# Optimization experiments

Measured on AMD Instinct MI355X. Metric: run time of the kernel, lower is better.

Reference implementation:

```python
import jax, jax.numpy as jnp
import numpy as np


def _decode(fm):
    # fm: [B, A, H, W, 5+C] YOLO head output
    B, A, H, W, D = fm.shape
    box = fm[..., :4].reshape(B, -1, 4)
    conf = jax.nn.sigmoid(fm[..., 4].reshape(B, -1))
    cls = jax.nn.sigmoid(fm[..., 5:].reshape(B, -1, D - 5))
    # Faithful to the torch in-place sequence:
    #   b0 = (b0 - b2/2)*W ; b1 = (b1 - b3/2)*H
    #   b2 = (NEW b0 + OLD b2/2)*W ; b3 = (NEW b1 + OLD b3/2)*H
    w = jnp.asarray(W, fm.dtype)
    h = jnp.asarray(H, fm.dtype)
    x1 = (box[..., 0] - box[..., 2] / 2) * w
    y1 = (box[..., 1] - box[..., 3] / 2) * h
    x2 = (x1 + box[..., 2] / 2) * w
    y2 = (y1 + box[..., 3] / 2) * h
    boxes = jnp.stack([x1, y1, x2, y2], axis=-1)  # [B, A*H*W, 4]
    return boxes, conf, cls


def setup_inputs() -> dict:
    key = jax.random.key(0)
    k0, k1, k2, k3 = jax.random.split(key, 4)
    B, A, C = 16, 3, 80
    fm0 = jax.random.uniform(k0, (B, A, 80, 80, 5 + C), dtype=jnp.float32)
    fm1 = jax.random.uniform(k1, (B, A, 40, 40, 5 + C), dtype=jnp.float32)
    fm2 = jax.random.uniform(k2, (B, A, 20, 20, 5 + C), dtype=jnp.float32)
    detection_targets = jax.random.uniform(k3, (1, 4), dtype=jnp.float32)
    return {"fm0": fm0, "fm1": fm1, "fm2": fm2,
            "detection_targets": detection_targets}


def reference(fm0, fm1, fm2, detection_targets):
    boxes, scores, classes = [], [], []
    for fm in (fm0, fm1, fm2):
        b, s, c = _decode(fm)
        boxes.append(b)
        scores.append(s)
        classes.append(c)
    all_boxes = jnp.concatenate(boxes, axis=1)    # [B, N, 4]
    all_scores = jnp.concatenate(scores, axis=1)  # [B, N]
    all_classes = jnp.concatenate(classes, axis=1)  # [B, N, C]
    # Pack like the torch nms_input: [x1, y1, x2, y2, conf, cls...]
    return jnp.concatenate(
        [all_boxes, all_scores[..., None], all_classes], axis=-1)  # [B, N, 5+C]
```

## Files before the change

### kernel.cpp

```cpp
#include <hip/hip_runtime.h>

#define NROWS_OUT 25200
#define L0_FLOATS 26112000
#define L1_FLOATS 6528000
#define L2_FLOATS 1632000
#define TOTAL_FLOATS (L0_FLOATS + L1_FLOATS + L2_FLOATS)
#define TOTAL4   (TOTAL_FLOATS / 4)
#define HALF4    (TOTAL4 / 2)

typedef float v4f __attribute__((ext_vector_type(4)));

__device__ __forceinline__ float fast_sigmoid(float x) {
    float e = __expf(-x);
    return __builtin_amdgcn_rcpf(1.0f + e);
}

template <int ROWS, int OFF, int SCALE>
__device__ __forceinline__ void process4(const float* __restrict__ in,
                                         float* __restrict__ out,
                                         int f_local) {
    constexpr int ROWS85 = ROWS * 85;
    const int b   = f_local / ROWS85;
    const int rem = f_local - b * ROWS85;
    const int c0  = rem % 85;

    int g = f_local;
    if (c0 <= 3)  g = f_local - c0;
    if (c0 >= 82) g = f_local + (85 - c0);

    const v4f x = *(const v4f*)(in + f_local);
    const float r0 = in[g + 0];
    const float r1 = in[g + 1];
    const float r2 = in[g + 2];
    const float r3 = in[g + 3];

    const float sc = (float)SCALE;
    const float h2 = 0.5f * r2, h3 = 0.5f * r3;
    const float q0 = (r0 - h2) * sc;
    const float q1 = (r1 - h3) * sc;
    const float q2 = (q0 + h2) * sc;
    const float q3 = (q1 + h3) * sc;

    float xv[4] = {x.x, x.y, x.z, x.w};
    float y[4];
#pragma unroll
    for (int k = 0; k < 4; ++k) {
        int c = c0 + k;
        if (c >= 85) c -= 85;
        const float s = fast_sigmoid(xv[k]);
        const float q = (c == 0) ? q0 : ((c == 1) ? q1 : ((c == 2) ? q2 : q3));
        y[k] = (c < 4) ? q : s;
    }

    const int out_f = (b * NROWS_OUT + OFF) * 85 + rem;
    v4f yo; yo.x = y[0]; yo.y = y[1]; yo.z = y[2]; yo.w = y[3];
    __builtin_nontemporal_store(yo, (v4f*)(out + out_f));
}

__device__ __forceinline__ void dispatch4(const float* __restrict__ fm0,
                                          const float* __restrict__ fm1,
                                          const float* __restrict__ fm2,
                                          float* __restrict__ out, int f) {
    if (f < L0_FLOATS) {
        process4<19200, 0, 80>(fm0, out, f);
    } else if (f < L0_FLOATS + L1_FLOATS) {
        process4<4800, 19200, 40>(fm1, out, f - L0_FLOATS);
    } else {
        process4<1200, 24000, 20>(fm2, out, f - (L0_FLOATS + L1_FLOATS));
    }
}

__global__ __launch_bounds__(256) void yolo_decode_kernel(
    const float* __restrict__ fm0, const float* __restrict__ fm1,
    const float* __restrict__ fm2, float* __restrict__ out) {
    const int v = blockIdx.x * 256 + threadIdx.x;
    if (v >= HALF4) return;
    dispatch4(fm0, fm1, fm2, out, v * 4);
    dispatch4(fm0, fm1, fm2, out, (v + HALF4) * 4);
}

extern "C" void kernel_launch(void* const* d_in, const int* in_sizes, int n_in,
                              void* d_out, int out_size, void* d_ws, size_t ws_size,
                              hipStream_t stream) {
    const float* fm0 = (const float*)d_in[0];
    const float* fm1 = (const float*)d_in[1];
    const float* fm2 = (const float*)d_in[2];
    float* out = (float*)d_out;

    const int blocks = (HALF4 + 255) / 256;
    hipLaunchKernelGGL(yolo_decode_kernel, dim3(blocks), dim3(256), 0, stream,
                       fm0, fm1, fm2, out);
}
```

Measured before the change: 236.3 us.

## Split decode into bulk sigmoid stream kernel and per-row box fixup kernel

```diff
diff --git a/kernel.cpp b/kernel.cpp
--- a/kernel.cpp
+++ b/kernel.cpp
@@ -1,12 +1,17 @@
 #include <hip/hip_runtime.h>
 
 #define NROWS_OUT 25200
+#define ROWS0 19200
+#define ROWS1 4800
+#define ROWS2 1200
+#define NB 16
 #define L0_FLOATS 26112000
 #define L1_FLOATS 6528000
 #define L2_FLOATS 1632000
 #define TOTAL_FLOATS (L0_FLOATS + L1_FLOATS + L2_FLOATS)
 #define TOTAL4   (TOTAL_FLOATS / 4)
 #define HALF4    (TOTAL4 / 2)
+#define NROWS_TOT (NB * NROWS_OUT)
 
 typedef float v4f __attribute__((ext_vector_type(4)));
 
@@ -15,24 +20,53 @@
     return __builtin_amdgcn_rcpf(1.0f + e);
 }
 
+template <int ROWS, int OFF>
+__device__ __forceinline__ void stream4(const float* __restrict__ in,
+                                        float* __restrict__ out,
+                                        int f_local) {
+    constexpr int ROWS85 = ROWS * 85;
+    const int b = f_local / ROWS85;
+    const v4f x = *(const v4f*)(in + f_local);
+    v4f y;
+    y.x = fast_sigmoid(x.x);
+    y.y = fast_sigmoid(x.y);
+    y.z = fast_sigmoid(x.z);
+    y.w = fast_sigmoid(x.w);
+    const int out_f = f_local + (b * (NROWS_OUT - ROWS) + OFF) * 85;
+    __builtin_nontemporal_store(y, (v4f*)(out + out_f));
+}
+
+__device__ __forceinline__ void sdispatch(const float* __restrict__ fm0,
+                                          const float* __restrict__ fm1,
+                                          const float* __restrict__ fm2,
+                                          float* __restrict__ out, int f) {
+    if (f < L0_FLOATS) {
+        stream4<ROWS0, 0>(fm0, out, f);
+    } else if (f < L0_FLOATS + L1_FLOATS) {
+        stream4<ROWS1, ROWS0>(fm1, out, f - L0_FLOATS);
+    } else {
+        stream4<ROWS2, ROWS0 + ROWS1>(fm2, out, f - (L0_FLOATS + L1_FLOATS));
+    }
+}
+
+__global__ __launch_bounds__(256) void yolo_sigmoid_kernel(
+    const float* __restrict__ fm0, const float* __restrict__ fm1,
+    const float* __restrict__ fm2, float* __restrict__ out) {
+    const int v = blockIdx.x * 256 + threadIdx.x;
+    if (v >= HALF4) return;
+    sdispatch(fm0, fm1, fm2, out, v * 4);
+    sdispatch(fm0, fm1, fm2, out, (v + HALF4) * 4);
+}
+
 template <int ROWS, int OFF, int SCALE>
-__device__ __forceinline__ void process4(const float* __restrict__ in,
-                                         float* __restrict__ out,
-                                         int f_local) {
-    constexpr int ROWS85 = ROWS * 85;
-    const int b   = f_local / ROWS85;
-    const int rem = f_local - b * ROWS85;
-    const int c0  = rem % 85;
-
-    int g = f_local;
-    if (c0 <= 3)  g = f_local - c0;
-    if (c0 >= 82) g = f_local + (85 - c0);
-
-    const v4f x = *(const v4f*)(in + f_local);
-    const float r0 = in[g + 0];
-    const float r1 = in[g + 1];
-    const float r2 = in[g + 2];
-    const float r3 = in[g + 3];
+__device__ __forceinline__ void fixrow(const float* __restrict__ in,
+                                       float* __restrict__ out, int tloc) {
+    const int b = tloc / ROWS;
+    const int gin = tloc * 85;
+    const float r0 = in[gin + 0];
+    const float r1 = in[gin + 1];
+    const float r2 = in[gin + 2];
+    const float r3 = in[gin + 3];
 
     const float sc = (float)SCALE;
     const float h2 = 0.5f * r2, h3 = 0.5f * r3;
@@ -41,42 +75,25 @@
     const float q2 = (q0 + h2) * sc;
     const float q3 = (q1 + h3) * sc;
 
-    float xv[4] = {x.x, x.y, x.z, x.w};
-    float y[4];
-#pragma unroll
-    for (int k = 0; k < 4; ++k) {
-        int c = c0 + k;
-        if (c >= 85) c -= 85;
-        const float s = fast_sigmoid(xv[k]);
-        const float q = (c == 0) ? q0 : ((c == 1) ? q1 : ((c == 2) ? q2 : q3));
-        y[k] = (c < 4) ? q : s;
-    }
-
-    const int out_f = (b * NROWS_OUT + OFF) * 85 + rem;
-    v4f yo; yo.x = y[0]; yo.y = y[1]; yo.z = y[2]; yo.w = y[3];
-    __builtin_nontemporal_store(yo, (v4f*)(out + out_f));
+    const int gout = (tloc + b * (NROWS_OUT - ROWS) + OFF) * 85;
+    out[gout + 0] = q0;
+    out[gout + 1] = q1;
+    out[gout + 2] = q2;
+    out[gout + 3] = q3;
 }
 
-__device__ __forceinline__ void dispatch4(const float* __restrict__ fm0,
-                                          const float* __restrict__ fm1,
-                                          const float* __restrict__ fm2,
-                                          float* __restrict__ out, int f) {
-    if (f < L0_FLOATS) {
-        process4<19200, 0, 80>(fm0, out, f);
-    } else if (f < L0_FLOATS + L1_FLOATS) {
-        process4<4800, 19200, 40>(fm1, out, f - L0_FLOATS);
-    } else {
-        process4<1200, 24000, 20>(fm2, out, f - (L0_FLOATS + L1_FLOATS));
-    }
-}
-
-__global__ __launch_bounds__(256) void yolo_decode_kernel(
+__global__ __launch_bounds__(256) void yolo_boxfix_kernel(
     const float* __restrict__ fm0, const float* __restrict__ fm1,
     const float* __restrict__ fm2, float* __restrict__ out) {
-    const int v = blockIdx.x * 256 + threadIdx.x;
-    if (v >= HALF4) return;
-    dispatch4(fm0, fm1, fm2, out, v * 4);
-    dispatch4(fm0, fm1, fm2, out, (v + HALF4) * 4);
+    const int t = blockIdx.x * 256 + threadIdx.x;
+    if (t >= NROWS_TOT) return;
+    if (t < NB * ROWS0) {
+        fixrow<ROWS0, 0, 80>(fm0, out, t);
+    } else if (t < NB * (ROWS0 + ROWS1)) {
+        fixrow<ROWS1, ROWS0, 40>(fm1, out, t - NB * ROWS0);
+    } else {
+        fixrow<ROWS2, ROWS0 + ROWS1, 20>(fm2, out, t - NB * (ROWS0 + ROWS1));
+    }
 }
 
 extern "C" void kernel_launch(void* const* d_in, const int* in_sizes, int n_in,
@@ -87,7 +104,11 @@
     const float* fm2 = (const float*)d_in[2];
     float* out = (float*)d_out;
 
-    const int blocks = (HALF4 + 255) / 256;
-    hipLaunchKernelGGL(yolo_decode_kernel, dim3(blocks), dim3(256), 0, stream,
+    const int blocks1 = (HALF4 + 255) / 256;
+    hipLaunchKernelGGL(yolo_sigmoid_kernel, dim3(blocks1), dim3(256), 0, stream,
+                       fm0, fm1, fm2, out);
+
+    const int blocks2 = (NROWS_TOT + 255) / 256;
+    hipLaunchKernelGGL(yolo_boxfix_kernel, dim3(blocks2), dim3(256), 0, stream,
                        fm0, fm1, fm2, out);
 }
```

After: 284.0 us. +20.2%, slower.

## Process four float4 chunks per thread with shared column decode and vector neighbor loads

Applied to the files above, without the earlier changes.

```diff
diff --git a/kernel.cpp b/kernel.cpp
--- a/kernel.cpp
+++ b/kernel.cpp
@@ -6,13 +6,63 @@
 #define L2_FLOATS 1632000
 #define TOTAL_FLOATS (L0_FLOATS + L1_FLOATS + L2_FLOATS)
 #define TOTAL4   (TOTAL_FLOATS / 4)
-#define HALF4    (TOTAL4 / 2)
+#define Q4       (TOTAL4 / 4)
+#define Q4F      (Q4 * 4)
+#define R85_0    1632000
+#define STEP_REM 408000
+#define OUT85    (NROWS_OUT * 85)
+#define Q3FASTV  102000
 
 typedef float v4f __attribute__((ext_vector_type(4)));
 
 __device__ __forceinline__ float fast_sigmoid(float x) {
     float e = __expf(-x);
     return __builtin_amdgcn_rcpf(1.0f + e);
+}
+
+__device__ __forceinline__ float pick(int c, float q0, float q1, float q2,
+                                      float q3, float s) {
+    const float q = (c == 0) ? q0 : ((c == 1) ? q1 : ((c == 2) ? q2 : q3));
+    return (c < 4) ? q : s;
+}
+
+struct Sel {
+    bool prevN, i1, i2;
+    int cc0, cc1, cc2, cc3;
+};
+
+template <int SCALE>
+__device__ __forceinline__ v4f decode4(const v4f x, const v4f n, const Sel s) {
+    const float w0 = s.prevN ? n.x : x.x;
+    const float w1 = s.prevN ? n.y : x.y;
+    const float w2 = s.prevN ? n.z : x.z;
+    const float w3 = s.prevN ? n.w : x.w;
+    const float w4 = s.prevN ? x.x : n.x;
+    const float w5 = s.prevN ? x.y : n.y;
+    const float w6 = s.prevN ? x.z : n.z;
+    const float a0 = s.i2 ? w2 : w0;
+    const float a1 = s.i2 ? w3 : w1;
+    const float a2 = s.i2 ? w4 : w2;
+    const float a3 = s.i2 ? w5 : w3;
+    const float a4 = s.i2 ? w6 : w4;
+    const float r0 = s.i1 ? a1 : a0;
+    const float r1 = s.i1 ? a2 : a1;
+    const float r2 = s.i1 ? a3 : a2;
+    const float r3 = s.i1 ? a4 : a3;
+
+    const float sc = (float)SCALE;
+    const float h2 = 0.5f * r2, h3 = 0.5f * r3;
+    const float q0 = (r0 - h2) * sc;
+    const float q1 = (r1 - h3) * sc;
+    const float q2 = (q0 + h2) * sc;
+    const float q3 = (q1 + h3) * sc;
+
+    v4f y;
+    y.x = pick(s.cc0, q0, q1, q2, q3, fast_sigmoid(x.x));
+    y.y = pick(s.cc1, q0, q1, q2, q3, fast_sigmoid(x.y));
+    y.z = pick(s.cc2, q0, q1, q2, q3, fast_sigmoid(x.z));
+    y.w = pick(s.cc3, q0, q1, q2, q3, fast_sigmoid(x.w));
+    return y;
 }
 
 template <int ROWS, int OFF, int SCALE>
@@ -24,46 +74,34 @@
     const int rem = f_local - b * ROWS85;
     const int c0  = rem % 85;
 
-    int g = f_local;
-    if (c0 <= 3)  g = f_local - c0;
-    if (c0 >= 82) g = f_local + (85 - c0);
+    const bool prevNeeded = (c0 >= 1) && (c0 <= 3);
+    const bool nextNeeded = (c0 >= 82);
+    int nb = f_local;
+    if (prevNeeded) nb = f_local - 4;
+    if (nextNeeded) nb = f_local + 4;
 
     const v4f x = *(const v4f*)(in + f_local);
-    const float r0 = in[g + 0];
-    const float r1 = in[g + 1];
-    const float r2 = in[g + 2];
-    const float r3 = in[g + 3];
+    const v4f n = *(const v4f*)(in + nb);
 
-    const float sc = (float)SCALE;
-    const float h2 = 0.5f * r2, h3 = 0.5f * r3;
-    const float q0 = (r0 - h2) * sc;
-    const float q1 = (r1 - h3) * sc;
-    const float q2 = (q0 + h2) * sc;
-    const float q3 = (q1 + h3) * sc;
+    Sel s;
+    s.prevN = prevNeeded;
+    const int idx = prevNeeded ? (4 - c0) : (nextNeeded ? (85 - c0) : 0);
+    s.i1 = (idx & 1) != 0;
+    s.i2 = (idx & 2) != 0;
+    int c1 = c0 + 1; if (c1 >= 85) c1 -= 85;
+    int c2 = c0 + 2; if (c2 >= 85) c2 -= 85;
+    int c3 = c0 + 3; if (c3 >= 85) c3 -= 85;
+    s.cc0 = c0; s.cc1 = c1; s.cc2 = c2; s.cc3 = c3;
 
-    float xv[4] = {x.x, x.y, x.z, x.w};
-    float y[4];
-#pragma unroll
-    for (int k = 0; k < 4; ++k) {
-        int c = c0 + k;
-        if (c >= 85) c -= 85;
-        const float s = fast_sigmoid(xv[k]);
-        const float q = (c == 0) ? q0 : ((c == 1) ? q1 : ((c == 2) ? q2 : q3));
-        y[k] = (c < 4) ? q : s;
-    }
-
+    const v4f y = decode4<SCALE>(x, n, s);
     const int out_f = (b * NROWS_OUT + OFF) * 85 + rem;
-    v4f yo; yo.x = y[0]; yo.y = y[1]; yo.z = y[2]; yo.w = y[3];
-    __builtin_nontemporal_store(yo, (v4f*)(out + out_f));
+    __builtin_nontemporal_store(y, (v4f*)(out + out_f));
 }
 
-__device__ __forceinline__ void dispatch4(const float* __restrict__ fm0,
-                                          const float* __restrict__ fm1,
-                                          const float* __restrict__ fm2,
-                                          float* __restrict__ out, int f) {
-    if (f < L0_FLOATS) {
-        process4<19200, 0, 80>(fm0, out, f);
-    } else if (f < L0_FLOATS + L1_FLOATS) {
+__device__ __forceinline__ void dispatch_slow(const float* __restrict__ fm1,
+                                              const float* __restrict__ fm2,
+                                              float* __restrict__ out, int f) {
+    if (f < L0_FLOATS + L1_FLOATS) {
         process4<4800, 19200, 40>(fm1, out, f - L0_FLOATS);
     } else {
         process4<1200, 24000, 20>(fm2, out, f - (L0_FLOATS + L1_FLOATS));
@@ -74,9 +112,60 @@
     const float* __restrict__ fm0, const float* __restrict__ fm1,
     const float* __restrict__ fm2, float* __restrict__ out) {
     const int v = blockIdx.x * 256 + threadIdx.x;
-    if (v >= HALF4) return;
-    dispatch4(fm0, fm1, fm2, out, v * 4);
-    dispatch4(fm0, fm1, fm2, out, (v + HALF4) * 4);
+    if (v >= Q4) return;
+
+    const int f0   = v * 4;
+    const int b0   = f0 / R85_0;
+    const int rem0 = f0 - b0 * R85_0;
+    const int c0   = rem0 % 85;
+
+    Sel s;
+    s.prevN = (c0 >= 1) && (c0 <= 3);
+    const bool nextN = (c0 >= 82);
+    const int dnb = s.prevN ? -4 : (nextN ? 4 : 0);
+    const int idx = s.prevN ? (4 - c0) : (nextN ? (85 - c0) : 0);
+    s.i1 = (idx & 1) != 0;
+    s.i2 = (idx & 2) != 0;
+    int c1 = c0 + 1; if (c1 >= 85) c1 -= 85;
+    int c2 = c0 + 2; if (c2 >= 85) c2 -= 85;
+    int c3 = c0 + 3; if (c3 >= 85) c3 -= 85;
+    s.cc0 = c0; s.cc1 = c1; s.cc2 = c2; s.cc3 = c3;
+
+    int b1 = b0 + 5, rem1 = rem0 + STEP_REM;
+    if (rem1 >= R85_0) { rem1 -= R85_0; ++b1; }
+    int b2 = b1 + 5, rem2 = rem1 + STEP_REM;
+    if (rem2 >= R85_0) { rem2 -= R85_0; ++b2; }
+
+    const int f1 = f0 + Q4F;
+    const int f2 = f0 + 2 * Q4F;
+    const int f3 = f0 + 3 * Q4F;
+    const bool q3fast = (v < Q3FASTV);
+
+    const v4f x0 = *(const v4f*)(fm0 + f0);
+    const v4f n0 = *(const v4f*)(fm0 + f0 + dnb);
+    const v4f x1 = *(const v4f*)(fm0 + f1);
+    const v4f n1 = *(const v4f*)(fm0 + f1 + dnb);
+    const v4f x2 = *(const v4f*)(fm0 + f2);
+    const v4f n2 = *(const v4f*)(fm0 + f2 + dnb);
+    v4f x3{}, n3{};
+    if (q3fast) {
+        x3 = *(const v4f*)(fm0 + f3);
+        n3 = *(const v4f*)(fm0 + f3 + dnb);
+    }
+
+    const v4f y0 = decode4<80>(x0, n0, s);
+    __builtin_nontemporal_store(y0, (v4f*)(out + b0 * OUT85 + rem0));
+    const v4f y1 = decode4<80>(x1, n1, s);
+    __builtin_nontemporal_store(y1, (v4f*)(out + b1 * OUT85 + rem1));
+    const v4f y2 = decode4<80>(x2, n2, s);
+    __builtin_nontemporal_store(y2, (v4f*)(out + b2 * OUT85 + rem2));
+    if (q3fast) {
+        const v4f y3 = decode4<80>(x3, n3, s);
+        __builtin_nontemporal_store(
+            y3, (v4f*)(out + 15 * OUT85 + (f0 + 1224000)));
+    } else {
+        dispatch_slow(fm1, fm2, out, f3);
+    }
 }
 
 extern "C" void kernel_launch(void* const* d_in, const int* in_sizes, int n_in,
@@ -87,7 +176,7 @@
     const float* fm2 = (const float*)d_in[2];
     float* out = (float*)d_out;
 
-    const int blocks = (HALF4 + 255) / 256;
+    const int blocks = (Q4 + 255) / 256;
     hipLaunchKernelGGL(yolo_decode_kernel, dim3(blocks), dim3(256), 0, stream,
                        fm0, fm1, fm2, out);
 }
```

Result: slower. 246.3 us (+4.2%).
